# Performance work log

Hardware: AMD Instinct MI355X
Metric: run time of the kernel (lower is better)

## Reference

```python
import jax, jax.numpy as jnp
import numpy as np
import random

EPS = 1e-16  # matches EKM eps default
B, M, N, R = 8, 8192, 512, 256


def setup_inputs() -> dict:
    key = jax.random.key(0)
    kx, = jax.random.split(key, 1)
    x = jax.random.normal(kx, (B, M, N), dtype=jnp.float32)
    # EKM init: random.seed(42); inds = random.sample(range(M), R)
    random.seed(42)
    inds = jnp.asarray(random.sample(range(M), R), dtype=jnp.int32)
    # EKMInit overrides ekm.alpha with nn.Parameter(torch.tensor([0.1]))
    alpha = jnp.asarray([0.1], dtype=jnp.float32)
    return {"x": x, "alpha": alpha, "inds": inds}


def _memberships(x, v, alpha):
    x2 = jnp.sum(x * x, axis=2, keepdims=True)           # (B, M, 1)
    xv = jnp.einsum('bmn,bnr->bmr', x, v)                # (B, M, R)
    v2 = jnp.sum(v * v, axis=1, keepdims=True)           # (B, 1, R)
    d = jax.nn.relu(x2 - 2.0 * xv + v2)
    return jax.nn.softmax(-d / alpha, axis=2)            # (B, M, R)


def reference(x, alpha, inds):
    # init: v0 = t(x[:, inds, :]) -> (B, N, R); u0 = memberships(x, v0)
    v0 = jnp.swapaxes(x[:, inds, :], 1, 2)               # (B, N, R)
    # solver step (num_iters=1): u_new = memberships(x, v0) (== u0),
    # v_new = centers(x, u_new)
    u = _memberships(x, v0, alpha)                       # (B, M, R)
    u_n = (u + EPS) / (jnp.sum(u, axis=1, keepdims=True) + EPS)
    v = jnp.einsum('bmn,bmr->bnr', x, u_n)               # (B, N, R)
    return (u, v)
```

## Files before the change

kernel.cpp:

```cpp
#include <hip/hip_runtime.h>
#include <math.h>

#define B 8
#define M 8192
#define N 512
#define R 256
#define EPSF 1e-16f

typedef __attribute__((ext_vector_type(8))) short short8;
typedef __attribute__((ext_vector_type(16))) float f32x16;

__device__ __forceinline__ unsigned short bf16_rtn(float f) {
    unsigned int u = __float_as_uint(f);
    u += 0x7FFFu + ((u >> 16) & 1u);
    return (unsigned short)(u >> 16);
}

__device__ __forceinline__ void gll16(const unsigned short* g, unsigned short* l) {
    __builtin_amdgcn_global_load_lds(
        (const __attribute__((address_space(1))) unsigned int*)g,
        (__attribute__((address_space(3))) unsigned int*)l, 16, 0, 0);
}

__global__ __launch_bounds__(256) void ekm_kc(
    const float* __restrict__ x, const int* __restrict__ inds,
    unsigned short* __restrict__ c_hi, unsigned short* __restrict__ c_lo,
    float* __restrict__ v2g)
{
    const int t = threadIdx.x, b = blockIdx.y;
    const int r = blockIdx.x * 16 + (t >> 4);
    const int seg = (t & 15) * 32;
    const float* src = x + ((size_t)b * M + inds[r]) * N + seg;
    unsigned short* hd = c_hi + ((size_t)b * R + r) * 512 + seg;
    unsigned short* ld = c_lo + ((size_t)b * R + r) * 512 + seg;
    float vp = 0.f;
#pragma unroll
    for (int c = 0; c < 4; ++c) {
        float4 f0 = *(const float4*)(src + c * 8);
        float4 f1 = *(const float4*)(src + c * 8 + 4);
        float av[8] = {f0.x, f0.y, f0.z, f0.w, f1.x, f1.y, f1.z, f1.w};
        unsigned ph[4], pl[4];
#pragma unroll
        for (int j = 0; j < 4; ++j) {
            vp += av[2*j] * av[2*j] + av[2*j+1] * av[2*j+1];
            unsigned short h0 = bf16_rtn(av[2*j]), h1 = bf16_rtn(av[2*j+1]);
            float r0 = av[2*j]   - __uint_as_float((unsigned)h0 << 16);
            float r1 = av[2*j+1] - __uint_as_float((unsigned)h1 << 16);
            ph[j] = (unsigned)h0 | ((unsigned)h1 << 16);
            pl[j] = (unsigned)bf16_rtn(r0) | ((unsigned)bf16_rtn(r1) << 16);
        }
        *(uint4*)(hd + c * 8) = make_uint4(ph[0], ph[1], ph[2], ph[3]);
        *(uint4*)(ld + c * 8) = make_uint4(pl[0], pl[1], pl[2], pl[3]);
    }
    vp += __shfl_xor(vp, 1); vp += __shfl_xor(vp, 2);
    vp += __shfl_xor(vp, 4); vp += __shfl_xor(vp, 8);
    if ((t & 15) == 0) v2g[b * R + r] = vp;
}

__global__ __launch_bounds__(256, 3) void ekm_k1(
    const float* __restrict__ x, const float* __restrict__ alpha_p,
    const unsigned short* __restrict__ c_hi, const unsigned short* __restrict__ c_lo,
    const float* __restrict__ v2g, float* __restrict__ u_out,
    unsigned short* __restrict__ uT, unsigned short* __restrict__ xT,
    float* __restrict__ colsum)
{
    __shared__ unsigned short Ah[64 * 40], Al[64 * 40];
    __shared__ unsigned short Bh[256 * 32], Bl[256 * 32];
    __shared__ float x2s[64];
    __shared__ float redm[4][64], reds[4][64];

    const int t = threadIdx.x;
    const int b = blockIdx.y;
    const int m0 = blockIdx.x * 64;
    const int w = t >> 6, l = t & 63, col = l & 31, h5 = l >> 5;
    const int arow = t >> 2, kch = t & 3;

    const float* ax = x + ((size_t)b * M + m0 + arow) * N + kch * 8;
    const unsigned short* bhs = c_hi + ((size_t)b * R + (t >> 2)) * 512 + (t & 3) * 8;
    const unsigned short* bls = c_lo + ((size_t)b * R + (t >> 2)) * 512 + (t & 3) * 8;

    f32x16 acc[2][2];
    acc[0][0] = (f32x16)0.f; acc[0][1] = (f32x16)0.f;
    acc[1][0] = (f32x16)0.f; acc[1][1] = (f32x16)0.f;

    float x2p = 0.f;

    for (int k0 = 0; k0 < N; k0 += 32) {
        float4 a0 = *(const float4*)(ax + k0);
        float4 a1 = *(const float4*)(ax + k0 + 4);
        x2p += a0.x*a0.x + a0.y*a0.y + a0.z*a0.z + a0.w*a0.w
             + a1.x*a1.x + a1.y*a1.y + a1.z*a1.z + a1.w*a1.w;
        float av[8] = {a0.x, a0.y, a0.z, a0.w, a1.x, a1.y, a1.z, a1.w};
        unsigned ph[4], pl[4];
#pragma unroll
        for (int j = 0; j < 4; ++j) {
            unsigned short h0 = bf16_rtn(av[2*j]), h1 = bf16_rtn(av[2*j+1]);
            float r0 = av[2*j]   - __uint_as_float((unsigned)h0 << 16);
            float r1 = av[2*j+1] - __uint_as_float((unsigned)h1 << 16);
            ph[j] = (unsigned)h0 | ((unsigned)h1 << 16);
            pl[j] = (unsigned)bf16_rtn(r0) | ((unsigned)bf16_rtn(r1) << 16);
        }
        __syncthreads();
#pragma unroll
        for (int i = 0; i < 4; ++i) {
            gll16(bhs + k0 + i * (64 * 512), Bh + i * 2048 + t * 8);
            gll16(bls + k0 + i * (64 * 512), Bl + i * 2048 + t * 8);
        }
        *(uint4*)&Ah[arow * 40 + kch * 8] = make_uint4(ph[0], ph[1], ph[2], ph[3]);
        *(uint4*)&Al[arow * 40 + kch * 8] = make_uint4(pl[0], pl[1], pl[2], pl[3]);
        __syncthreads();

        {
            int kk = t >> 3, ms = (t & 7) * 8;
            unsigned q0 = (unsigned)Ah[(ms+0)*40+kk] | ((unsigned)Ah[(ms+1)*40+kk] << 16);
            unsigned q1 = (unsigned)Ah[(ms+2)*40+kk] | ((unsigned)Ah[(ms+3)*40+kk] << 16);
            unsigned q2 = (unsigned)Ah[(ms+4)*40+kk] | ((unsigned)Ah[(ms+5)*40+kk] << 16);
            unsigned q3 = (unsigned)Ah[(ms+6)*40+kk] | ((unsigned)Ah[(ms+7)*40+kk] << 16);
            *(uint4*)(xT + ((size_t)b * N + k0 + kk) * M + m0 + ms) = make_uint4(q0, q1, q2, q3);
        }

#pragma unroll
        for (int half = 0; half < 2; ++half) {
            short8 ah[2], al2[2], bh[2], bl2[2];
#pragma unroll
            for (int tm = 0; tm < 2; ++tm) {
                ah[tm]  = *(const short8*)&Ah[(tm*32 + col) * 40 + half*16 + h5*8];
                al2[tm] = *(const short8*)&Al[(tm*32 + col) * 40 + half*16 + h5*8];
            }
#pragma unroll
            for (int tr = 0; tr < 2; ++tr) {
                bh[tr]  = *(const short8*)&Bh[(w*64 + tr*32 + col) * 32 + half*16 + h5*8];
                bl2[tr] = *(const short8*)&Bl[(w*64 + tr*32 + col) * 32 + half*16 + h5*8];
            }
#pragma unroll
            for (int tm = 0; tm < 2; ++tm)
#pragma unroll
            for (int tr = 0; tr < 2; ++tr) {
                acc[tm][tr] = __builtin_amdgcn_mfma_f32_32x32x16_bf16(ah[tm],  bh[tr],  acc[tm][tr], 0, 0, 0);
                acc[tm][tr] = __builtin_amdgcn_mfma_f32_32x32x16_bf16(ah[tm],  bl2[tr], acc[tm][tr], 0, 0, 0);
                acc[tm][tr] = __builtin_amdgcn_mfma_f32_32x32x16_bf16(al2[tm], bh[tr],  acc[tm][tr], 0, 0, 0);
            }
        }
    }

    x2p += __shfl_xor(x2p, 1);
    x2p += __shfl_xor(x2p, 2);
    if (kch == 0) x2s[arow] = x2p;
    __syncthreads();

    const float ia = 1.4426950408889634f / alpha_p[0];
    float v2c[2];
#pragma unroll
    for (int tr = 0; tr < 2; ++tr)
        v2c[tr] = v2g[b * R + w * 64 + tr * 32 + col];

#pragma unroll
    for (int tm = 0; tm < 2; ++tm)
#pragma unroll
    for (int reg = 0; reg < 16; ++reg) {
        int rowl = (reg & 3) + 8 * (reg >> 2) + 4 * h5;
        float x2v = x2s[tm * 32 + rowl];
        float mn;
#pragma unroll
        for (int tr = 0; tr < 2; ++tr) {
            float d = x2v - 2.f * acc[tm][tr][reg] + v2c[tr];
            d = fmaxf(d, 0.f);
            acc[tm][tr][reg] = d;
            mn = (tr == 0) ? d : fminf(mn, d);
        }
        mn = fminf(mn, __shfl_xor(mn, 1));
        mn = fminf(mn, __shfl_xor(mn, 2));
        mn = fminf(mn, __shfl_xor(mn, 4));
        mn = fminf(mn, __shfl_xor(mn, 8));
        mn = fminf(mn, __shfl_xor(mn, 16));
        if (col == 0) redm[w][tm * 32 + rowl] = mn;
    }
    __syncthreads();

#pragma unroll
    for (int tm = 0; tm < 2; ++tm)
#pragma unroll
    for (int reg = 0; reg < 16; ++reg) {
        int m = tm * 32 + (reg & 3) + 8 * (reg >> 2) + 4 * h5;
        float mn = fminf(fminf(redm[0][m], redm[1][m]), fminf(redm[2][m], redm[3][m]));
        float s = 0.f;
#pragma unroll
        for (int tr = 0; tr < 2; ++tr) {
            float e = exp2f((mn - acc[tm][tr][reg]) * ia);
            acc[tm][tr][reg] = e;
            s += e;
        }
        s += __shfl_xor(s, 1); s += __shfl_xor(s, 2); s += __shfl_xor(s, 4);
        s += __shfl_xor(s, 8); s += __shfl_xor(s, 16);
        if (col == 0) reds[w][m] = s;
    }
    __syncthreads();

    float* ub = u_out + ((size_t)b * M + m0) * R + w * 64;
    float cs[2] = {0.f, 0.f};
#pragma unroll
    for (int tm = 0; tm < 2; ++tm)
#pragma unroll
    for (int reg = 0; reg < 16; ++reg) {
        int rowl = (reg & 3) + 8 * (reg >> 2) + 4 * h5;
        int m = tm * 32 + rowl;
        float inv = 1.f / (reds[0][m] + reds[1][m] + reds[2][m] + reds[3][m]);
#pragma unroll
        for (int tr = 0; tr < 2; ++tr) {
            float uu = acc[tm][tr][reg] * inv;
            acc[tm][tr][reg] = uu;
            ub[(size_t)m * R + tr * 32 + col] = uu;
            cs[tr] += uu;
        }
    }
    unsigned short* uTb = uT + ((size_t)b * R + w * 64) * M + m0;
#pragma unroll
    for (int tm = 0; tm < 2; ++tm)
#pragma unroll
    for (int tr = 0; tr < 2; ++tr)
#pragma unroll
    for (int rq = 0; rq < 4; ++rq) {
        uint2 p;
        p.x = (unsigned)bf16_rtn(acc[tm][tr][rq*4+0]) | ((unsigned)bf16_rtn(acc[tm][tr][rq*4+1]) << 16);
        p.y = (unsigned)bf16_rtn(acc[tm][tr][rq*4+2]) | ((unsigned)bf16_rtn(acc[tm][tr][rq*4+3]) << 16);
        *(uint2*)(uTb + (size_t)(tr*32 + col) * M + tm*32 + 8*rq + 4*h5) = p;
    }
    cs[0] += __shfl_xor(cs[0], 32);
    cs[1] += __shfl_xor(cs[1], 32);
    if (h5 == 0) {
        atomicAdd(&colsum[b * R + w * 64 + col], cs[0]);
        atomicAdd(&colsum[b * R + w * 64 + 32 + col], cs[1]);
    }
}

__global__ __launch_bounds__(256, 4) void ekm_k2(
    const unsigned short* __restrict__ xT, const unsigned short* __restrict__ uT,
    float* __restrict__ part)
{
    __shared__ unsigned short XA[128 * 32], UB[128 * 32];
    const int t = threadIdx.x;
    const int nt = blockIdx.x >> 1, rt = blockIdx.x & 1;
    const int slab = blockIdx.y, b = blockIdx.z;
    const int n0 = nt * 128, r0 = rt * 128;
    const int w = t >> 6, l = t & 63, col = l & 31, h5 = l >> 5;
    const int wn = w >> 1, wr = w & 1;

    const unsigned short* xs = xT + ((size_t)b * N + n0 + (t >> 2)) * M + slab * 1024 + (t & 3) * 8;
    const unsigned short* us = uT + ((size_t)b * R + r0 + (t >> 2)) * M + slab * 1024 + (t & 3) * 8;

    f32x16 acc[2][2];
    acc[0][0] = (f32x16)0.f; acc[0][1] = (f32x16)0.f;
    acc[1][0] = (f32x16)0.f; acc[1][1] = (f32x16)0.f;

    for (int k0 = 0; k0 < 1024; k0 += 32) {
        __syncthreads();
#pragma unroll
        for (int i = 0; i < 2; ++i) {
            gll16(xs + k0 + (size_t)i * 64 * M, XA + i * 2048 + t * 8);
            gll16(us + k0 + (size_t)i * 64 * M, UB + i * 2048 + t * 8);
        }
        __syncthreads();
#pragma unroll
        for (int half = 0; half < 2; ++half) {
            short8 af[2], bf2[2];
#pragma unroll
            for (int tm = 0; tm < 2; ++tm)
                af[tm] = *(const short8*)&XA[(wn*64 + tm*32 + col) * 32 + half*16 + h5*8];
#pragma unroll
            for (int tr = 0; tr < 2; ++tr)
                bf2[tr] = *(const short8*)&UB[(wr*64 + tr*32 + col) * 32 + half*16 + h5*8];
#pragma unroll
            for (int tm = 0; tm < 2; ++tm)
#pragma unroll
            for (int tr = 0; tr < 2; ++tr)
                acc[tm][tr] = __builtin_amdgcn_mfma_f32_32x32x16_bf16(af[tm], bf2[tr], acc[tm][tr], 0, 0, 0);
        }
    }

    float* pb = part + (size_t)slab * ((size_t)B * N * R) + (size_t)b * N * R;
#pragma unroll
    for (int tm = 0; tm < 2; ++tm)
#pragma unroll
    for (int reg = 0; reg < 16; ++reg) {
        int n = n0 + wn*64 + tm*32 + (reg & 3) + 8*(reg >> 2) + 4*h5;
#pragma unroll
        for (int tr = 0; tr < 2; ++tr)
            pb[(size_t)n * R + r0 + wr*64 + tr*32 + col] = acc[tm][tr][reg];
    }
}

__global__ __launch_bounds__(256) void ekm_red(
    const float* __restrict__ part, const float* __restrict__ colsum,
    float* __restrict__ v_out)
{
    size_t o = ((size_t)blockIdx.x * 256 + threadIdx.x) * 4;
    float sx = 0.f, sy = 0.f, sz = 0.f, sw = 0.f;
#pragma unroll
    for (int sl = 0; sl < 8; ++sl) {
        float4 p = *(const float4*)(part + (size_t)sl * B * N * R + o);
        sx += p.x; sy += p.y; sz += p.z; sw += p.w;
    }
    int b = (int)(o >> 17);
    int r = (int)(o & (R - 1));
    float4 cs = *(const float4*)(colsum + b * R + r);
    float4 vo;
    vo.x = sx / (cs.x + EPSF);
    vo.y = sy / (cs.y + EPSF);
    vo.z = sz / (cs.z + EPSF);
    vo.w = sw / (cs.w + EPSF);
    *(float4*)(v_out + o) = vo;
}

extern "C" void kernel_launch(void* const* d_in, const int* in_sizes, int n_in,
                              void* d_out, int out_size, void* d_ws, size_t ws_size,
                              hipStream_t stream) {
    const float* x     = (const float*)d_in[0];
    const float* alpha = (const float*)d_in[1];
    const int*   inds  = (const int*)d_in[2];

    float* u_out = (float*)d_out;
    float* v_out = u_out + (size_t)B * M * R;

    char* ws = (char*)d_ws;
    const size_t CH = (size_t)B * R * 512 * 2;
    unsigned short* c_hi   = (unsigned short*)ws;
    unsigned short* c_lo   = (unsigned short*)(ws + CH);
    float*          v2g    = (float*)(ws + 2 * CH);
    float*          colsum = (float*)(ws + 2 * CH + (size_t)B * R * 4);
    char* p = ws + 2 * CH + 2 * (size_t)B * R * 4;
    unsigned short* xT = (unsigned short*)p;          p += (size_t)B * N * M * 2;
    unsigned short* uT = (unsigned short*)p;          p += (size_t)B * R * M * 2;
    float*          part = (float*)p;

    hipMemsetAsync(colsum, 0, (size_t)B * R * sizeof(float), stream);

    ekm_kc<<<dim3(16, B), 256, 0, stream>>>(x, inds, c_hi, c_lo, v2g);
    ekm_k1<<<dim3(M / 64, B), 256, 0, stream>>>(x, alpha, c_hi, c_lo, v2g,
                                                u_out, uT, xT, colsum);
    ekm_k2<<<dim3(8, 8, B), 256, 0, stream>>>(xT, uT, part);
    ekm_red<<<(B * N * R / 4) / 256, 256, 0, stream>>>(part, colsum, v_out);
}
```

Baseline: 359.0 us.

## Restructure EKM kernels: direct B-fragment loads, separate transpose, unsplit K2 without reduction

In k1, the center (B) operand tiles are no longer staged through LDS. Each lane loads its MFMA fragments straight from global memory, and the next x slice is prefetched into registers. The xT transpose moves out of k1 into a dedicated LDS-tiled transpose kernel. k2 now covers the full M range with 64x64 tiles and an XOR-swizzled LDS layout, holds U fragments in registers, and applies the colsum normalisation before writing v directly, which removes the split-K partial buffer and the reduction kernel. The trade-offs are that k2 loses parallelism (fewer blocks, long serial K loop), and k1 issues uncoalesced global loads for the center data.

```diff
diff --git a/kernel.cpp b/kernel.cpp
--- a/kernel.cpp
+++ b/kernel.cpp
@@ -57,15 +57,42 @@
     if ((t & 15) == 0) v2g[b * R + r] = vp;
 }
 
+__global__ __launch_bounds__(256) void ekm_t(
+    const float* __restrict__ x, unsigned short* __restrict__ xT)
+{
+    __shared__ unsigned short S[64 * 130];
+    const int t = threadIdx.x;
+    const int m0 = blockIdx.x * 64, n0 = blockIdx.y * 128, b = blockIdx.z;
+#pragma unroll
+    for (int it = 0; it < 8; ++it) {
+        int idx = it * 256 + t;
+        int m = idx >> 5, c4 = idx & 31;
+        float4 v = *(const float4*)(x + ((size_t)b * M + m0 + m) * N + n0 + c4 * 4);
+        uint2 p;
+        p.x = (unsigned)bf16_rtn(v.x) | ((unsigned)bf16_rtn(v.y) << 16);
+        p.y = (unsigned)bf16_rtn(v.z) | ((unsigned)bf16_rtn(v.w) << 16);
+        *(uint2*)&S[m * 130 + c4 * 4] = p;
+    }
+    __syncthreads();
+#pragma unroll
+    for (int it = 0; it < 4; ++it) {
+        int idx = it * 256 + t;
+        int n = idx >> 3, mc = (idx & 7) * 8;
+        unsigned q[4];
+#pragma unroll
+        for (int j = 0; j < 4; ++j)
+            q[j] = (unsigned)S[(mc + 2*j) * 130 + n] | ((unsigned)S[(mc + 2*j + 1) * 130 + n] << 16);
+        *(uint4*)(xT + ((size_t)b * N + n0 + n) * M + m0 + mc) = make_uint4(q[0], q[1], q[2], q[3]);
+    }
+}
+
 __global__ __launch_bounds__(256, 3) void ekm_k1(
     const float* __restrict__ x, const float* __restrict__ alpha_p,
     const unsigned short* __restrict__ c_hi, const unsigned short* __restrict__ c_lo,
     const float* __restrict__ v2g, float* __restrict__ u_out,
-    unsigned short* __restrict__ uT, unsigned short* __restrict__ xT,
-    float* __restrict__ colsum)
+    unsigned short* __restrict__ uT, float* __restrict__ colsum)
 {
     __shared__ unsigned short Ah[64 * 40], Al[64 * 40];
-    __shared__ unsigned short Bh[256 * 32], Bl[256 * 32];
     __shared__ float x2s[64];
     __shared__ float redm[4][64], reds[4][64];
 
@@ -76,18 +103,19 @@
     const int arow = t >> 2, kch = t & 3;
 
     const float* ax = x + ((size_t)b * M + m0 + arow) * N + kch * 8;
-    const unsigned short* bhs = c_hi + ((size_t)b * R + (t >> 2)) * 512 + (t & 3) * 8;
-    const unsigned short* bls = c_lo + ((size_t)b * R + (t >> 2)) * 512 + (t & 3) * 8;
+    const size_t rowb = (size_t)(b * R + w * 64 + col) * 512 + h5 * 8;
+    const unsigned short* bh_p = c_hi + rowb;
+    const unsigned short* bl_p = c_lo + rowb;
 
     f32x16 acc[2][2];
     acc[0][0] = (f32x16)0.f; acc[0][1] = (f32x16)0.f;
     acc[1][0] = (f32x16)0.f; acc[1][1] = (f32x16)0.f;
 
     float x2p = 0.f;
+    float4 a0 = *(const float4*)(ax);
+    float4 a1 = *(const float4*)(ax + 4);
 
     for (int k0 = 0; k0 < N; k0 += 32) {
-        float4 a0 = *(const float4*)(ax + k0);
-        float4 a1 = *(const float4*)(ax + k0 + 4);
         x2p += a0.x*a0.x + a0.y*a0.y + a0.z*a0.z + a0.w*a0.w
              + a1.x*a1.x + a1.y*a1.y + a1.z*a1.z + a1.w*a1.w;
         float av[8] = {a0.x, a0.y, a0.z, a0.w, a1.x, a1.y, a1.z, a1.w};
@@ -101,45 +129,47 @@
             pl[j] = (unsigned)bf16_rtn(r0) | ((unsigned)bf16_rtn(r1) << 16);
         }
         __syncthreads();
-#pragma unroll
-        for (int i = 0; i < 4; ++i) {
-            gll16(bhs + k0 + i * (64 * 512), Bh + i * 2048 + t * 8);
-            gll16(bls + k0 + i * (64 * 512), Bl + i * 2048 + t * 8);
-        }
         *(uint4*)&Ah[arow * 40 + kch * 8] = make_uint4(ph[0], ph[1], ph[2], ph[3]);
         *(uint4*)&Al[arow * 40 + kch * 8] = make_uint4(pl[0], pl[1], pl[2], pl[3]);
         __syncthreads();
 
-        {
-            int kk = t >> 3, ms = (t & 7) * 8;
-            unsigned q0 = (unsigned)Ah[(ms+0)*40+kk] | ((unsigned)Ah[(ms+1)*40+kk] << 16);
-            unsigned q1 = (unsigned)Ah[(ms+2)*40+kk] | ((unsigned)Ah[(ms+3)*40+kk] << 16);
-            unsigned q2 = (unsigned)Ah[(ms+4)*40+kk] | ((unsigned)Ah[(ms+5)*40+kk] << 16);
-            unsigned q3 = (unsigned)Ah[(ms+6)*40+kk] | ((unsigned)Ah[(ms+7)*40+kk] << 16);
-            *(uint4*)(xT + ((size_t)b * N + k0 + kk) * M + m0 + ms) = make_uint4(q0, q1, q2, q3);
-        }
+        if (k0 + 32 < N) {
+            a0 = *(const float4*)(ax + k0 + 32);
+            a1 = *(const float4*)(ax + k0 + 36);
+        }
+
+        short8 bh[2][2], bl[2][2];
+#pragma unroll
+        for (int tr = 0; tr < 2; ++tr)
+#pragma unroll
+            for (int half = 0; half < 2; ++half) {
+                bh[tr][half] = *(const short8*)(bh_p + tr * 32 * 512 + k0 + half * 16);
+                bl[tr][half] = *(const short8*)(bl_p + tr * 32 * 512 + k0 + half * 16);
+            }
 
 #pragma unroll
         for (int half = 0; half < 2; ++half) {
-            short8 ah[2], al2[2], bh[2], bl2[2];
+            short8 ah[2], al2[2];
 #pragma unroll
             for (int tm = 0; tm < 2; ++tm) {
                 ah[tm]  = *(const short8*)&Ah[(tm*32 + col) * 40 + half*16 + h5*8];
                 al2[tm] = *(const short8*)&Al[(tm*32 + col) * 40 + half*16 + h5*8];
             }
 #pragma unroll
-            for (int tr = 0; tr < 2; ++tr) {
-                bh[tr]  = *(const short8*)&Bh[(w*64 + tr*32 + col) * 32 + half*16 + h5*8];
-                bl2[tr] = *(const short8*)&Bl[(w*64 + tr*32 + col) * 32 + half*16 + h5*8];
-            }
-#pragma unroll
             for (int tm = 0; tm < 2; ++tm)
 #pragma unroll
-            for (int tr = 0; tr < 2; ++tr) {
-                acc[tm][tr] = __builtin_amdgcn_mfma_f32_32x32x16_bf16(ah[tm],  bh[tr],  acc[tm][tr], 0, 0, 0);
-                acc[tm][tr] = __builtin_amdgcn_mfma_f32_32x32x16_bf16(ah[tm],  bl2[tr], acc[tm][tr], 0, 0, 0);
-                acc[tm][tr] = __builtin_amdgcn_mfma_f32_32x32x16_bf16(al2[tm], bh[tr],  acc[tm][tr], 0, 0, 0);
-            }
+            for (int tr = 0; tr < 2; ++tr)
+                acc[tm][tr] = __builtin_amdgcn_mfma_f32_32x32x16_bf16(ah[tm], bh[tr][half], acc[tm][tr], 0, 0, 0);
+#pragma unroll
+            for (int tm = 0; tm < 2; ++tm)
+#pragma unroll
+            for (int tr = 0; tr < 2; ++tr)
+                acc[tm][tr] = __builtin_amdgcn_mfma_f32_32x32x16_bf16(ah[tm], bl[tr][half], acc[tm][tr], 0, 0, 0);
+#pragma unroll
+            for (int tm = 0; tm < 2; ++tm)
+#pragma unroll
+            for (int tr = 0; tr < 2; ++tr)
+                acc[tm][tr] = __builtin_amdgcn_mfma_f32_32x32x16_bf16(al2[tm], bh[tr][half], acc[tm][tr], 0, 0, 0);
         }
     }
 
@@ -235,80 +265,49 @@
 
 __global__ __launch_bounds__(256, 4) void ekm_k2(
     const unsigned short* __restrict__ xT, const unsigned short* __restrict__ uT,
-    float* __restrict__ part)
+    const float* __restrict__ colsum, float* __restrict__ v_out)
 {
-    __shared__ unsigned short XA[128 * 32], UB[128 * 32];
+    __shared__ unsigned short XS[64 * 128];
     const int t = threadIdx.x;
-    const int nt = blockIdx.x >> 1, rt = blockIdx.x & 1;
-    const int slab = blockIdx.y, b = blockIdx.z;
-    const int n0 = nt * 128, r0 = rt * 128;
+    const int n0 = blockIdx.x * 64, r0 = blockIdx.y * 64, b = blockIdx.z;
     const int w = t >> 6, l = t & 63, col = l & 31, h5 = l >> 5;
     const int wn = w >> 1, wr = w & 1;
 
-    const unsigned short* xs = xT + ((size_t)b * N + n0 + (t >> 2)) * M + slab * 1024 + (t & 3) * 8;
-    const unsigned short* us = uT + ((size_t)b * R + r0 + (t >> 2)) * M + slab * 1024 + (t & 3) * 8;
-
-    f32x16 acc[2][2];
-    acc[0][0] = (f32x16)0.f; acc[0][1] = (f32x16)0.f;
-    acc[1][0] = (f32x16)0.f; acc[1][1] = (f32x16)0.f;
-
-    for (int k0 = 0; k0 < 1024; k0 += 32) {
+    const int schunk = (t & 15) ^ ((t >> 4) & 15);
+    const unsigned short* xs = xT + ((size_t)b * N + n0 + (t >> 4)) * M + schunk * 8;
+    const unsigned short* ub = uT + ((size_t)(b * R + r0 + wr * 32 + col)) * M + h5 * 8;
+
+    f32x16 acc0 = (f32x16)0.f, acc1 = (f32x16)0.f;
+
+    for (int k0 = 0; k0 < M; k0 += 128) {
         __syncthreads();
 #pragma unroll
-        for (int i = 0; i < 2; ++i) {
-            gll16(xs + k0 + (size_t)i * 64 * M, XA + i * 2048 + t * 8);
-            gll16(us + k0 + (size_t)i * 64 * M, UB + i * 2048 + t * 8);
-        }
+        for (int i = 0; i < 4; ++i)
+            gll16(xs + (size_t)i * 16 * M + k0, XS + i * 2048 + t * 8);
         __syncthreads();
-#pragma unroll
-        for (int half = 0; half < 2; ++half) {
-            short8 af[2], bf2[2];
-#pragma unroll
-            for (int tm = 0; tm < 2; ++tm)
-                af[tm] = *(const short8*)&XA[(wn*64 + tm*32 + col) * 32 + half*16 + h5*8];
-#pragma unroll
-            for (int tr = 0; tr < 2; ++tr)
-                bf2[tr] = *(const short8*)&UB[(wr*64 + tr*32 + col) * 32 + half*16 + h5*8];
-#pragma unroll
-            for (int tm = 0; tm < 2; ++tm)
-#pragma unroll
-            for (int tr = 0; tr < 2; ++tr)
-                acc[tm][tr] = __builtin_amdgcn_mfma_f32_32x32x16_bf16(af[tm], bf2[tr], acc[tm][tr], 0, 0, 0);
-        }
-    }
-
-    float* pb = part + (size_t)slab * ((size_t)B * N * R) + (size_t)b * N * R;
-#pragma unroll
-    for (int tm = 0; tm < 2; ++tm)
+
+        short8 bfrag[8];
+#pragma unroll
+        for (int g = 0; g < 8; ++g)
+            bfrag[g] = *(const short8*)(ub + k0 + g * 16);
+
+#pragma unroll
+        for (int g = 0; g < 8; ++g) {
+            const int pc = (2 * g + h5) ^ (col & 15);
+            short8 af = *(const short8*)&XS[(wn * 32 + col) * 128 + pc * 8];
+            if (g & 1)
+                acc1 = __builtin_amdgcn_mfma_f32_32x32x16_bf16(af, bfrag[g], acc1, 0, 0, 0);
+            else
+                acc0 = __builtin_amdgcn_mfma_f32_32x32x16_bf16(af, bfrag[g], acc0, 0, 0, 0);
+        }
+    }
+
+    const float inv = 1.f / (colsum[b * R + r0 + wr * 32 + col] + EPSF);
 #pragma unroll
     for (int reg = 0; reg < 16; ++reg) {
-        int n = n0 + wn*64 + tm*32 + (reg & 3) + 8*(reg >> 2) + 4*h5;
-#pragma unroll
-        for (int tr = 0; tr < 2; ++tr)
-            pb[(size_t)n * R + r0 + wr*64 + tr*32 + col] = acc[tm][tr][reg];
-    }
-}
-
-__global__ __launch_bounds__(256) void ekm_red(
-    const float* __restrict__ part, const float* __restrict__ colsum,
-    float* __restrict__ v_out)
-{
-    size_t o = ((size_t)blockIdx.x * 256 + threadIdx.x) * 4;
-    float sx = 0.f, sy = 0.f, sz = 0.f, sw = 0.f;
-#pragma unroll
-    for (int sl = 0; sl < 8; ++sl) {
-        float4 p = *(const float4*)(part + (size_t)sl * B * N * R + o);
-        sx += p.x; sy += p.y; sz += p.z; sw += p.w;
-    }
-    int b = (int)(o >> 17);
-    int r = (int)(o & (R - 1));
-    float4 cs = *(const float4*)(colsum + b * R + r);
-    float4 vo;
-    vo.x = sx / (cs.x + EPSF);
-    vo.y = sy / (cs.y + EPSF);
-    vo.z = sz / (cs.z + EPSF);
-    vo.w = sw / (cs.w + EPSF);
-    *(float4*)(v_out + o) = vo;
+        int n = n0 + wn * 32 + (reg & 3) + 8 * (reg >> 2) + 4 * h5;
+        v_out[((size_t)b * N + n) * R + r0 + wr * 32 + col] = (acc0[reg] + acc1[reg]) * inv;
+    }
 }
 
 extern "C" void kernel_launch(void* const* d_in, const int* in_sizes, int n_in,
@@ -329,14 +328,13 @@
     float*          colsum = (float*)(ws + 2 * CH + (size_t)B * R * 4);
     char* p = ws + 2 * CH + 2 * (size_t)B * R * 4;
     unsigned short* xT = (unsigned short*)p;          p += (size_t)B * N * M * 2;
-    unsigned short* uT = (unsigned short*)p;          p += (size_t)B * R * M * 2;
-    float*          part = (float*)p;
+    unsigned short* uT = (unsigned short*)p;
 
     hipMemsetAsync(colsum, 0, (size_t)B * R * sizeof(float), stream);
 
     ekm_kc<<<dim3(16, B), 256, 0, stream>>>(x, inds, c_hi, c_lo, v2g);
     ekm_k1<<<dim3(M / 64, B), 256, 0, stream>>>(x, alpha, c_hi, c_lo, v2g,
-                                                u_out, uT, xT, colsum);
-    ekm_k2<<<dim3(8, 8, B), 256, 0, stream>>>(xT, uT, part);
-    ekm_red<<<(B * N * R / 4) / 256, 256, 0, stream>>>(part, colsum, v_out);
-}
+                                                u_out, uT, colsum);
+    ekm_t<<<dim3(M / 64, N / 128, B), 256, 0, stream>>>(x, xT);
+    ekm_k2<<<dim3(N / 64, R / 64, B), 256, 0, stream>>>(xT, uT, colsum, v_out);
+}
```

Result: slower. 472.4 us (+31.6%).
